# Kernel tuning notes

Measured on AMD Instinct MI355X. Metric: run time of the kernel, lower is better.

## Reference

```python
import jax, jax.numpy as jnp
import numpy as np

N, E_DIM, T = 32, 512, 2048
N_E = 8192
BETA = 0.25

def setup_inputs() -> dict:
    key = jax.random.key(0)
    k1, k2 = jax.random.split(key)
    z = jax.random.normal(k1, (N, E_DIM, T), dtype=jnp.float32)
    # nn.Embedding weight initialized uniform(-1/n_e, 1/n_e)
    emb = jax.random.uniform(k2, (N_E, E_DIM), dtype=jnp.float32,
                             minval=-1.0 / N_E, maxval=1.0 / N_E)
    return {"z": z, "emb": emb}

def reference(z, emb):
    n, width, t = z.shape
    # preprocess: (N, C, T) -> (N, T, C) -> (N*T, C)
    zf = jnp.transpose(z, (0, 2, 1)).reshape(-1, width)  # [M, e_dim]
    # squared euclidean distances: ||z||^2 + ||e||^2 - 2 z e^T
    d = (jnp.sum(zf ** 2, axis=1, keepdims=True)
         + jnp.sum(emb ** 2, axis=1)
         - 2.0 * jnp.matmul(zf, emb.T))  # [M, n_e]
    idx = jnp.argmin(d, axis=1)  # [M]
    z_q = emb[idx]  # [M, e_dim]
    sg = jax.lax.stop_gradient
    loss = jnp.mean((z_q - sg(zf)) ** 2) + BETA * jnp.mean((sg(z_q) - zf) ** 2)
    # straight-through estimator
    z_q = zf + sg(z_q - zf)
    # (N*T, C) -> (N, T, C) -> (N, C, T)
    z_q = jnp.transpose(z_q.reshape(n, t, width), (0, 2, 1))
    # perplexity from codebook usage histogram
    one_hot = jax.nn.one_hot(idx, emb.shape[0], dtype=zf.dtype)  # [M, n_e]
    e_mean = jnp.mean(one_hot, axis=0)
    perplexity = jnp.exp(-jnp.sum(e_mean * jnp.log(e_mean + 1e-10)))
    return (z_q, loss, perplexity)
```

## Files before the change

kernel.cpp:

```cpp
#include <hip/hip_runtime.h>
#include <stdint.h>

#define NE 8192
#define KD 512
#define MT 65536

typedef __attribute__((ext_vector_type(8))) short bf16x8;
typedef __attribute__((ext_vector_type(4))) float f32x4;

union U128 { uint4 u; bf16x8 b; };

#define WS_SUMZ2   0
#define WS_SUMSMIN 4
#define WS_HIST    8
#define WS_ZEROSZ  40960
#define WS_E2      40960
#define WS_IDX     73728
#define WS_EMB16   335872
#define WS_Z16     8724480

__device__ __forceinline__ unsigned int f2bf(float f) {
    union { float f; unsigned int u; } c; c.f = f;
    return (c.u + 0x7FFFu + ((c.u >> 16) & 1u)) >> 16;
}

__device__ __forceinline__ void load_lds16(const void* g, void* l) {
    __builtin_amdgcn_global_load_lds((const __attribute__((address_space(1))) void*)g,
                                     (__attribute__((address_space(3))) void*)l,
                                     16, 0, 0);
}

__global__ void k_embprep(const float* __restrict__ emb,
                          unsigned short* __restrict__ emb16,
                          float* __restrict__ e2) {
    const int code = blockIdx.x;
    const int lane = threadIdx.x;
    const float4* row = (const float4*)(emb + (size_t)code * KD);
    float4 a = row[lane * 2];
    float4 b = row[lane * 2 + 1];
    float s = a.x*a.x + a.y*a.y + a.z*a.z + a.w*a.w
            + b.x*b.x + b.y*b.y + b.z*b.z + b.w*b.w;
    uint4 o;
    o.x = f2bf(a.x) | (f2bf(a.y) << 16);
    o.y = f2bf(a.z) | (f2bf(a.w) << 16);
    o.z = f2bf(b.x) | (f2bf(b.y) << 16);
    o.w = f2bf(b.z) | (f2bf(b.w) << 16);
    ((uint4*)(emb16 + (size_t)code * KD))[lane] = o;
    #pragma unroll
    for (int off = 32; off; off >>= 1) s += __shfl_down(s, off, 64);
    if (lane == 0) e2[code] = s;
}

__global__ void k_zprep(const float* __restrict__ z,
                        unsigned short* __restrict__ z16,
                        float* __restrict__ sumz2) {
    __shared__ float arr[64][65];
    __shared__ float red[4];
    const int tid = threadIdx.x;
    const int n  = blockIdx.z;
    const int c0 = blockIdx.y * 64;
    const int t0 = blockIdx.x * 64;
    const int tl = tid & 63;
    const int cw = tid >> 6;
    const float* base = z + ((size_t)n * KD + c0) * 2048 + t0;
    float s = 0.f;
    #pragma unroll
    for (int u = 0; u < 16; u++) {
        int c = u * 4 + cw;
        float v = base[(size_t)c * 2048 + tl];
        arr[c][tl] = v;
        s += v * v;
    }
    #pragma unroll
    for (int off = 32; off; off >>= 1) s += __shfl_down(s, off, 64);
    if (tl == 0) red[cw] = s;
    __syncthreads();
    if (tid == 0) atomicAdd(sumz2, red[0] + red[1] + red[2] + red[3]);
    #pragma unroll
    for (int iter = 0; iter < 2; iter++) {
        int task = iter * 256 + tid;
        int row = task >> 3;
        int ch  = task & 7;
        float f0 = arr[ch*8+0][row], f1 = arr[ch*8+1][row],
              f2v = arr[ch*8+2][row], f3 = arr[ch*8+3][row],
              f4 = arr[ch*8+4][row], f5 = arr[ch*8+5][row],
              f6 = arr[ch*8+6][row], f7 = arr[ch*8+7][row];
        uint4 o;
        o.x = f2bf(f0) | (f2bf(f1) << 16);
        o.y = f2bf(f2v) | (f2bf(f3) << 16);
        o.z = f2bf(f4) | (f2bf(f5) << 16);
        o.w = f2bf(f6) | (f2bf(f7) << 16);
        *(uint4*)(z16 + ((size_t)(n * 2048 + t0 + row)) * KD + c0 + ch * 8) = o;
    }
}

__global__ __launch_bounds__(512, 2) void k_main(
    const unsigned short* __restrict__ z16,
    const unsigned short* __restrict__ emb16,
    const float* __restrict__ e2,
    int* __restrict__ g_idx,
    int* __restrict__ hist,
    float* __restrict__ sums)
{
    __shared__ __align__(16) unsigned short zt[128 * 512];
    __shared__ __align__(16) unsigned short et[2][256 * 32];

    const int tid  = threadIdx.x;
    const int lane = tid & 63;
    const int w    = tid >> 6;
    const int wm   = w & 1;
    const int wn   = w >> 1;
    const int quad = lane >> 4;
    const int col  = lane & 15;
    const int m0   = blockIdx.x * 128;

    {
        const int r  = tid >> 2;
        const int jb = (tid & 3) << 4;
        const uint4* gz = (const uint4*)(z16 + (size_t)(m0 + r) * KD);
        uint4* zt4w = (uint4*)zt;
        #pragma unroll
        for (int jj = 0; jj < 16; jj++) {
            int j  = jb + jj;
            int js = (j & 56) | ((j ^ r) & 7);
            zt4w[r * 64 + js] = gz[j];
        }
    }

    const int st_nl0 = w * 16 + (lane >> 2);
    const int st_q   = ((lane & 3) - ((st_nl0 >> 1) & 3)) & 3;
    const int st_q8  = st_q * 8;
    unsigned short* st_l0 = &et[0][0] + w * 512 + lane * 8;
    unsigned short* st_l1 = &et[0][0] + 4096 + w * 512 + lane * 8;

    f32x4 acc[4][4];
    #pragma unroll
    for (int mf = 0; mf < 4; mf++)
        #pragma unroll
        for (int nf = 0; nf < 4; nf++)
            acc[mf][nf] = (f32x4){0.f, 0.f, 0.f, 0.f};

    float rbv[4][4]; int rbi[4][4];
    #pragma unroll
    for (int mf = 0; mf < 4; mf++)
        #pragma unroll
        for (int rg = 0; rg < 4; rg++) { rbv[mf][rg] = 3.0e38f; rbi[mf][rg] = 0; }

    int zbase[4], r7[4];
    #pragma unroll
    for (int mf = 0; mf < 4; mf++) {
        int r = wm * 64 + mf * 16 + col;
        zbase[mf] = r * 64;
        r7[mf] = r & 7;
    }
    int bidx[4];
    #pragma unroll
    for (int nf = 0; nf < 4; nf++) {
        int nn = wn * 64 + nf * 16 + col;
        bidx[nf] = nn * 4 + ((quad + (nn >> 1)) & 3);
    }

    const uint4* zt4 = (const uint4*)zt;
    const uint4* et4[2] = { (const uint4*)&et[0][0], (const uint4*)&et[1][0] };

    {
        const unsigned short* g0 = emb16 + ((size_t)(st_nl0) << 9) + st_q8;
        const unsigned short* g1 = emb16 + ((size_t)(128 + st_nl0) << 9) + st_q8;
        load_lds16(g0, st_l0);
        load_lds16(g1, st_l1);
    }

    #pragma unroll 1
    for (int chunk = 0; chunk < 32; chunk++) {
        #pragma unroll
        for (int kk = 0; kk < 16; kk++) {
            __syncthreads();
            const int nxt = chunk * 16 + kk + 1;
            if (nxt < 512) {
                const int nchunk = nxt >> 4, nkk = nxt & 15, nbuf = nxt & 1;
                const size_t koff = (size_t)nkk * 32 + st_q8;
                const unsigned short* g0 = emb16 + (((size_t)(nchunk * 256 + st_nl0)) << 9) + koff;
                const unsigned short* g1 = emb16 + (((size_t)(nchunk * 256 + 128 + st_nl0)) << 9) + koff;
                load_lds16(g0, st_l0 + nbuf * 8192);
                load_lds16(g1, st_l1 + nbuf * 8192);
            }
            const int buf = kk & 1;
            const int jhi  = (kk * 4) & 56;
            const int jlow = ((kk & 1) << 2) | quad;
            bf16x8 af[4], bfv[4];
            #pragma unroll
            for (int mf = 0; mf < 4; mf++) {
                U128 u; u.u = zt4[zbase[mf] + (jhi | (jlow ^ r7[mf]))];
                af[mf] = u.b;
            }
            #pragma unroll
            for (int nf = 0; nf < 4; nf++) {
                U128 u; u.u = et4[buf][bidx[nf]];
                bfv[nf] = u.b;
            }
            #pragma unroll
            for (int mf = 0; mf < 4; mf++)
                #pragma unroll
                for (int nf = 0; nf < 4; nf++)
                    acc[mf][nf] = __builtin_amdgcn_mfma_f32_16x16x32_bf16(
                        af[mf], bfv[nf], acc[mf][nf], 0, 0, 0);
        }
        const int nb = chunk * 256 + wn * 64 + col;
        float e2v[4];
        #pragma unroll
        for (int nf = 0; nf < 4; nf++) e2v[nf] = e2[nb + nf * 16];
        #pragma unroll
        for (int mf = 0; mf < 4; mf++) {
            #pragma unroll
            for (int rg = 0; rg < 4; rg++) {
                float v0 = fmaf(-2.f, acc[mf][0][rg], e2v[0]);
                float v1 = fmaf(-2.f, acc[mf][1][rg], e2v[1]);
                float v2 = fmaf(-2.f, acc[mf][2][rg], e2v[2]);
                float v3 = fmaf(-2.f, acc[mf][3][rg], e2v[3]);
                float bv = v0; int bn = 0;
                if (v1 < bv) { bv = v1; bn = 1; }
                if (v2 < bv) { bv = v2; bn = 2; }
                if (v3 < bv) { bv = v3; bn = 3; }
                if (bv < rbv[mf][rg]) { rbv[mf][rg] = bv; rbi[mf][rg] = nb + (bn << 4); }
            }
            #pragma unroll
            for (int nf = 0; nf < 4; nf++)
                acc[mf][nf] = (f32x4){0.f, 0.f, 0.f, 0.f};
        }
    }

    #pragma unroll
    for (int mf = 0; mf < 4; mf++) {
        #pragma unroll
        for (int rg = 0; rg < 4; rg++) {
            float bv = rbv[mf][rg]; int bi = rbi[mf][rg];
            #pragma unroll
            for (int off = 1; off < 16; off <<= 1) {
                float ov = __shfl_xor(bv, off, 64);
                int   oi = __shfl_xor(bi, off, 64);
                if (ov < bv || (ov == bv && oi < bi)) { bv = ov; bi = oi; }
            }
            rbv[mf][rg] = bv; rbi[mf][rg] = bi;
        }
    }

    __syncthreads();
    float* sv = (float*)&et[0][0];
    int*   si = (int*)(sv + 512);
    if (col == 0) {
        #pragma unroll
        for (int mf = 0; mf < 4; mf++)
            #pragma unroll
            for (int rg = 0; rg < 4; rg++) {
                int rl = wm * 64 + mf * 16 + quad * 4 + rg;
                sv[wn * 128 + rl] = rbv[mf][rg];
                si[wn * 128 + rl] = rbi[mf][rg];
            }
    }
    __syncthreads();
    float myv = 0.f;
    if (tid < 128) {
        float bv = sv[tid]; int bi = si[tid];
        #pragma unroll
        for (int wnn = 1; wnn < 4; wnn++) {
            float ov = sv[wnn * 128 + tid]; int oi = si[wnn * 128 + tid];
            if (ov < bv || (ov == bv && oi < bi)) { bv = ov; bi = oi; }
        }
        g_idx[m0 + tid] = bi;
        atomicAdd(&hist[bi], 1);
        myv = bv;
    }
    #pragma unroll
    for (int off = 32; off; off >>= 1) myv += __shfl_down(myv, off, 64);
    if (lane == 0 && w < 2) atomicAdd(&sums[1], myv);
}

__global__ void k_final(const int* __restrict__ hist,
                        const float* __restrict__ sums,
                        float* __restrict__ out_scalars) {
    __shared__ float red[4];
    const int tid = threadIdx.x;
    float s = 0.f;
    for (int i = tid; i < NE; i += 256) {
        float e = (float)hist[i] * (1.0f / 65536.0f);
        s += e * logf(e + 1e-10f);
    }
    #pragma unroll
    for (int off = 32; off; off >>= 1) s += __shfl_down(s, off, 64);
    if ((tid & 63) == 0) red[tid >> 6] = s;
    __syncthreads();
    if (tid == 0) {
        float total = red[0] + red[1] + red[2] + red[3];
        float perp = expf(-total);
        float loss = 1.25f * (sums[0] + sums[1]) / (65536.0f * 512.0f);
        out_scalars[0] = loss;
        out_scalars[1] = perp;
    }
}

__global__ void k_gather(const float* __restrict__ emb,
                         const int* __restrict__ idx,
                         float* __restrict__ out) {
    __shared__ int ids[256];
    const int n  = blockIdx.y;
    const int t0 = blockIdx.x * 256;
    const int tid = threadIdx.x;
    ids[tid] = idx[n * 2048 + t0 + tid];
    __syncthreads();
    const int tq = tid & 63;
    const int cg = tid >> 6;
    const float* e0 = emb + (size_t)ids[tq * 4 + 0] * KD;
    const float* e1 = emb + (size_t)ids[tq * 4 + 1] * KD;
    const float* e2p = emb + (size_t)ids[tq * 4 + 2] * KD;
    const float* e3 = emb + (size_t)ids[tq * 4 + 3] * KD;
    for (int cb = cg * 4; cb < KD; cb += 16) {
        float4 a = *(const float4*)(e0 + cb);
        float4 b = *(const float4*)(e1 + cb);
        float4 c = *(const float4*)(e2p + cb);
        float4 d = *(const float4*)(e3 + cb);
        float* op = out + ((size_t)(n * KD + cb)) * 2048 + t0 + tq * 4;
        float4 o0 = {a.x, b.x, c.x, d.x};
        float4 o1 = {a.y, b.y, c.y, d.y};
        float4 o2 = {a.z, b.z, c.z, d.z};
        float4 o3 = {a.w, b.w, c.w, d.w};
        *(float4*)(op)        = o0;
        *(float4*)(op + 2048) = o1;
        *(float4*)(op + 4096) = o2;
        *(float4*)(op + 6144) = o3;
    }
}

extern "C" void kernel_launch(void* const* d_in, const int* in_sizes, int n_in,
                              void* d_out, int out_size, void* d_ws, size_t ws_size,
                              hipStream_t stream) {
    (void)in_sizes; (void)n_in; (void)out_size; (void)ws_size;
    const float* z   = (const float*)d_in[0];
    const float* emb = (const float*)d_in[1];
    float* out = (float*)d_out;
    char* ws = (char*)d_ws;

    float*          sums  = (float*)(ws + WS_SUMZ2);
    int*            hist  = (int*)(ws + WS_HIST);
    float*          e2    = (float*)(ws + WS_E2);
    int*            g_idx = (int*)(ws + WS_IDX);
    unsigned short* emb16 = (unsigned short*)(ws + WS_EMB16);
    unsigned short* z16   = (unsigned short*)(ws + WS_Z16);

    hipMemsetAsync(ws, 0, WS_ZEROSZ, stream);

    k_embprep<<<NE, 64, 0, stream>>>(emb, emb16, e2);
    k_zprep<<<dim3(32, 8, 32), 256, 0, stream>>>(z, z16, sums);
    k_main<<<512, 512, 0, stream>>>(z16, emb16, e2, g_idx, hist, sums);
    k_final<<<1, 256, 0, stream>>>(hist, sums, out + 33554432);
    k_gather<<<dim3(8, 32), 256, 0, stream>>>(emb, g_idx, out);
}
```

Before: 919.3 us.

## Software-pipeline codebook staging through registers and prefetch LDS fragments

Replaces the direct global-to-LDS loads of codebook tiles with a four-deep register ring of plain global loads that are written into the double-buffered LDS a couple of steps later. The A and B fragments for the next k-step are read from LDS before the current MFMA block runs, and the MFMAs are wrapped in s_setprio. The e2 loads for the epilogue are hoisted into the k-loop. The aim is to hide global and LDS latency behind MFMA work and cut barrier stalls, at the cost of more VGPRs. The z-prep kernel separately switches to float4 loads.

```diff
diff --git a/kernel.cpp b/kernel.cpp
--- a/kernel.cpp
+++ b/kernel.cpp
@@ -22,12 +22,6 @@
 __device__ __forceinline__ unsigned int f2bf(float f) {
     union { float f; unsigned int u; } c; c.f = f;
     return (c.u + 0x7FFFu + ((c.u >> 16) & 1u)) >> 16;
-}
-
-__device__ __forceinline__ void load_lds16(const void* g, void* l) {
-    __builtin_amdgcn_global_load_lds((const __attribute__((address_space(1))) void*)g,
-                                     (__attribute__((address_space(3))) void*)l,
-                                     16, 0, 0);
 }
 
 __global__ void k_embprep(const float* __restrict__ emb,
@@ -60,20 +54,21 @@
     const int n  = blockIdx.z;
     const int c0 = blockIdx.y * 64;
     const int t0 = blockIdx.x * 64;
-    const int tl = tid & 63;
-    const int cw = tid >> 6;
+    const int tl4 = (tid & 15) * 4;
+    const int cw  = tid >> 4;
     const float* base = z + ((size_t)n * KD + c0) * 2048 + t0;
     float s = 0.f;
     #pragma unroll
-    for (int u = 0; u < 16; u++) {
-        int c = u * 4 + cw;
-        float v = base[(size_t)c * 2048 + tl];
-        arr[c][tl] = v;
-        s += v * v;
+    for (int u = 0; u < 4; u++) {
+        int c = u * 16 + cw;
+        float4 v = *(const float4*)(base + (size_t)c * 2048 + tl4);
+        arr[c][tl4 + 0] = v.x; arr[c][tl4 + 1] = v.y;
+        arr[c][tl4 + 2] = v.z; arr[c][tl4 + 3] = v.w;
+        s += v.x*v.x + v.y*v.y + v.z*v.z + v.w*v.w;
     }
     #pragma unroll
     for (int off = 32; off; off >>= 1) s += __shfl_down(s, off, 64);
-    if (tl == 0) red[cw] = s;
+    if ((tid & 63) == 0) red[tid >> 6] = s;
     __syncthreads();
     if (tid == 0) atomicAdd(sumz2, red[0] + red[1] + red[2] + red[3]);
     #pragma unroll
@@ -114,6 +109,12 @@
     const int col  = lane & 15;
     const int m0   = blockIdx.x * 128;
 
+    const int st_nl0 = w * 16 + (lane >> 2);
+    const int st_q8  = ((((lane & 3) - ((st_nl0 >> 1) & 3)) & 3)) * 8;
+    unsigned short* st_l0 = &et[0][0] + w * 512 + lane * 8;
+    const unsigned short* gst0 = emb16 + ((size_t)st_nl0 << 9) + st_q8;
+    const unsigned short* gst1 = gst0 + (128 << 9);
+
     {
         const int r  = tid >> 2;
         const int jb = (tid & 3) << 4;
@@ -127,11 +128,15 @@
         }
     }
 
-    const int st_nl0 = w * 16 + (lane >> 2);
-    const int st_q   = ((lane & 3) - ((st_nl0 >> 1) & 3)) & 3;
-    const int st_q8  = st_q * 8;
-    unsigned short* st_l0 = &et[0][0] + w * 512 + lane * 8;
-    unsigned short* st_l1 = &et[0][0] + 4096 + w * 512 + lane * 8;
+    uint4 sg0[4], sg1[4];
+    uint4 p00 = *(const uint4*)(gst0);
+    uint4 p01 = *(const uint4*)(gst1);
+    uint4 p10 = *(const uint4*)(gst0 + 32);
+    uint4 p11 = *(const uint4*)(gst1 + 32);
+    sg0[2] = *(const uint4*)(gst0 + 64);
+    sg1[2] = *(const uint4*)(gst1 + 64);
+    sg0[3] = *(const uint4*)(gst0 + 96);
+    sg1[3] = *(const uint4*)(gst1 + 96);
 
     f32x4 acc[4][4];
     #pragma unroll
@@ -160,63 +165,85 @@
         bidx[nf] = nn * 4 + ((quad + (nn >> 1)) & 3);
     }
 
+    *(uint4*)st_l0 = p00;
+    *(uint4*)(st_l0 + 4096) = p01;
+    *(uint4*)(st_l0 + 8192) = p10;
+    *(uint4*)(st_l0 + 12288) = p11;
+    asm volatile("s_waitcnt lgkmcnt(0)" ::: "memory");
+    __builtin_amdgcn_s_barrier();
+
     const uint4* zt4 = (const uint4*)zt;
-    const uint4* et4[2] = { (const uint4*)&et[0][0], (const uint4*)&et[1][0] };
-
-    {
-        const unsigned short* g0 = emb16 + ((size_t)(st_nl0) << 9) + st_q8;
-        const unsigned short* g1 = emb16 + ((size_t)(128 + st_nl0) << 9) + st_q8;
-        load_lds16(g0, st_l0);
-        load_lds16(g1, st_l1);
+
+    bf16x8 af[2][4], bfv[2][4];
+    #pragma unroll
+    for (int mf = 0; mf < 4; mf++) {
+        U128 u; u.u = zt4[zbase[mf] + (quad ^ r7[mf])];
+        af[0][mf] = u.b;
+    }
+    #pragma unroll
+    for (int nf = 0; nf < 4; nf++) {
+        U128 u; u.u = ((const uint4*)&et[0][0])[bidx[nf]];
+        bfv[0][nf] = u.b;
     }
 
     #pragma unroll 1
     for (int chunk = 0; chunk < 32; chunk++) {
+        float e2v0, e2v1, e2v2, e2v3;
         #pragma unroll
         for (int kk = 0; kk < 16; kk++) {
-            __syncthreads();
-            const int nxt = chunk * 16 + kk + 1;
-            if (nxt < 512) {
-                const int nchunk = nxt >> 4, nkk = nxt & 15, nbuf = nxt & 1;
-                const size_t koff = (size_t)nkk * 32 + st_q8;
-                const unsigned short* g0 = emb16 + (((size_t)(nchunk * 256 + st_nl0)) << 9) + koff;
-                const unsigned short* g1 = emb16 + (((size_t)(nchunk * 256 + 128 + st_nl0)) << 9) + koff;
-                load_lds16(g0, st_l0 + nbuf * 8192);
-                load_lds16(g1, st_l1 + nbuf * 8192);
-            }
-            const int buf = kk & 1;
-            const int jhi  = (kk * 4) & 56;
-            const int jlow = ((kk & 1) << 2) | quad;
-            bf16x8 af[4], bfv[4];
-            #pragma unroll
-            for (int mf = 0; mf < 4; mf++) {
-                U128 u; u.u = zt4[zbase[mf] + (jhi | (jlow ^ r7[mf]))];
-                af[mf] = u.b;
-            }
-            #pragma unroll
-            for (int nf = 0; nf < 4; nf++) {
-                U128 u; u.u = et4[buf][bidx[nf]];
-                bfv[nf] = u.b;
-            }
+            const int g = chunk * 16 + kk;
+            {
+                int s = g + 4; if (s > 511) s = 511;
+                const size_t off = (((size_t)(s >> 4)) << 17) + (size_t)((s & 15) * 32);
+                sg0[kk & 3] = *(const uint4*)(gst0 + off);
+                sg1[kk & 3] = *(const uint4*)(gst1 + off);
+            }
+            {
+                const int kk1 = (kk + 1) & 15;
+                const int jhi = (kk1 * 4) & 56;
+                const int jlow = ((kk1 & 1) << 2) | quad;
+                const uint4* etp = (const uint4*)&et[(kk + 1) & 1][0];
+                #pragma unroll
+                for (int mf = 0; mf < 4; mf++) {
+                    U128 u; u.u = zt4[zbase[mf] + (jhi | (jlow ^ r7[mf]))];
+                    af[(kk + 1) & 1][mf] = u.b;
+                }
+                #pragma unroll
+                for (int nf = 0; nf < 4; nf++) {
+                    U128 u; u.u = etp[bidx[nf]];
+                    bfv[(kk + 1) & 1][nf] = u.b;
+                }
+            }
+            {
+                unsigned short* d0 = st_l0 + ((kk & 1) << 13);
+                *(uint4*)d0 = sg0[(kk + 2) & 3];
+                *(uint4*)(d0 + 4096) = sg1[(kk + 2) & 3];
+            }
+            if (kk == 14) {
+                const int nbv = chunk * 256 + wn * 64 + col;
+                e2v0 = e2[nbv];      e2v1 = e2[nbv + 16];
+                e2v2 = e2[nbv + 32]; e2v3 = e2[nbv + 48];
+            }
+            __builtin_amdgcn_s_setprio(1);
             #pragma unroll
             for (int mf = 0; mf < 4; mf++)
                 #pragma unroll
                 for (int nf = 0; nf < 4; nf++)
                     acc[mf][nf] = __builtin_amdgcn_mfma_f32_16x16x32_bf16(
-                        af[mf], bfv[nf], acc[mf][nf], 0, 0, 0);
+                        af[kk & 1][mf], bfv[kk & 1][nf], acc[mf][nf], 0, 0, 0);
+            __builtin_amdgcn_s_setprio(0);
+            asm volatile("s_waitcnt lgkmcnt(0)" ::: "memory");
+            __builtin_amdgcn_s_barrier();
         }
         const int nb = chunk * 256 + wn * 64 + col;
-        float e2v[4];
-        #pragma unroll
-        for (int nf = 0; nf < 4; nf++) e2v[nf] = e2[nb + nf * 16];
         #pragma unroll
         for (int mf = 0; mf < 4; mf++) {
             #pragma unroll
             for (int rg = 0; rg < 4; rg++) {
-                float v0 = fmaf(-2.f, acc[mf][0][rg], e2v[0]);
-                float v1 = fmaf(-2.f, acc[mf][1][rg], e2v[1]);
-                float v2 = fmaf(-2.f, acc[mf][2][rg], e2v[2]);
-                float v3 = fmaf(-2.f, acc[mf][3][rg], e2v[3]);
+                float v0 = fmaf(-2.f, acc[mf][0][rg], e2v0);
+                float v1 = fmaf(-2.f, acc[mf][1][rg], e2v1);
+                float v2 = fmaf(-2.f, acc[mf][2][rg], e2v2);
+                float v3 = fmaf(-2.f, acc[mf][3][rg], e2v3);
                 float bv = v0; int bn = 0;
                 if (v1 < bv) { bv = v1; bn = 1; }
                 if (v2 < bv) { bv = v2; bn = 2; }
```

Result: slower. 1.403 ms (+52.6%).

## Software-pipeline z fragment loads, prefetch e2, and vectorize zprep loads

Applied to the files above, without the earlier changes.

The main distance GEMM loop now double-buffers the A-operand (z) fragments in registers, loading the next k-step's fragments before issuing the current MFMAs. The barrier moves to the end of each iteration. Codebook norms e2 are prefetched during the second-to-last k-step so the per-chunk argmin does not stall on a global load. MFMA issue is bracketed with s_setprio to favour the matrix work, and the z preprocessing kernel switches to float4 global loads. The register double buffer raises VGPR pressure, which may lower occupancy.

```diff
diff --git a/kernel.cpp b/kernel.cpp
--- a/kernel.cpp
+++ b/kernel.cpp
@@ -60,20 +60,21 @@
     const int n  = blockIdx.z;
     const int c0 = blockIdx.y * 64;
     const int t0 = blockIdx.x * 64;
-    const int tl = tid & 63;
-    const int cw = tid >> 6;
+    const int tl4 = (tid & 15) * 4;
+    const int cw  = tid >> 4;
     const float* base = z + ((size_t)n * KD + c0) * 2048 + t0;
     float s = 0.f;
     #pragma unroll
-    for (int u = 0; u < 16; u++) {
-        int c = u * 4 + cw;
-        float v = base[(size_t)c * 2048 + tl];
-        arr[c][tl] = v;
-        s += v * v;
+    for (int u = 0; u < 4; u++) {
+        int c = u * 16 + cw;
+        float4 v = *(const float4*)(base + (size_t)c * 2048 + tl4);
+        arr[c][tl4 + 0] = v.x; arr[c][tl4 + 1] = v.y;
+        arr[c][tl4 + 2] = v.z; arr[c][tl4 + 3] = v.w;
+        s += v.x*v.x + v.y*v.y + v.z*v.z + v.w*v.w;
     }
     #pragma unroll
     for (int off = 32; off; off >>= 1) s += __shfl_down(s, off, 64);
-    if (tl == 0) red[cw] = s;
+    if ((tid & 63) == 0) red[tid >> 6] = s;
     __syncthreads();
     if (tid == 0) atomicAdd(sumz2, red[0] + red[1] + red[2] + red[3]);
     #pragma unroll
@@ -133,36 +134,6 @@
     unsigned short* st_l0 = &et[0][0] + w * 512 + lane * 8;
     unsigned short* st_l1 = &et[0][0] + 4096 + w * 512 + lane * 8;
 
-    f32x4 acc[4][4];
-    #pragma unroll
-    for (int mf = 0; mf < 4; mf++)
-        #pragma unroll
-        for (int nf = 0; nf < 4; nf++)
-            acc[mf][nf] = (f32x4){0.f, 0.f, 0.f, 0.f};
-
-    float rbv[4][4]; int rbi[4][4];
-    #pragma unroll
-    for (int mf = 0; mf < 4; mf++)
-        #pragma unroll
-        for (int rg = 0; rg < 4; rg++) { rbv[mf][rg] = 3.0e38f; rbi[mf][rg] = 0; }
-
-    int zbase[4], r7[4];
-    #pragma unroll
-    for (int mf = 0; mf < 4; mf++) {
-        int r = wm * 64 + mf * 16 + col;
-        zbase[mf] = r * 64;
-        r7[mf] = r & 7;
-    }
-    int bidx[4];
-    #pragma unroll
-    for (int nf = 0; nf < 4; nf++) {
-        int nn = wn * 64 + nf * 16 + col;
-        bidx[nf] = nn * 4 + ((quad + (nn >> 1)) & 3);
-    }
-
-    const uint4* zt4 = (const uint4*)zt;
-    const uint4* et4[2] = { (const uint4*)&et[0][0], (const uint4*)&et[1][0] };
-
     {
         const unsigned short* g0 = emb16 + ((size_t)(st_nl0) << 9) + st_q8;
         const unsigned short* g1 = emb16 + ((size_t)(128 + st_nl0) << 9) + st_q8;
@@ -170,11 +141,51 @@
         load_lds16(g1, st_l1);
     }
 
+    f32x4 acc[4][4];
+    #pragma unroll
+    for (int mf = 0; mf < 4; mf++)
+        #pragma unroll
+        for (int nf = 0; nf < 4; nf++)
+            acc[mf][nf] = (f32x4){0.f, 0.f, 0.f, 0.f};
+
+    float rbv[4][4]; int rbi[4][4];
+    #pragma unroll
+    for (int mf = 0; mf < 4; mf++)
+        #pragma unroll
+        for (int rg = 0; rg < 4; rg++) { rbv[mf][rg] = 3.0e38f; rbi[mf][rg] = 0; }
+
+    int zbase[4], r7[4];
+    #pragma unroll
+    for (int mf = 0; mf < 4; mf++) {
+        int r = wm * 64 + mf * 16 + col;
+        zbase[mf] = r * 64;
+        r7[mf] = r & 7;
+    }
+    int bidx[4];
+    #pragma unroll
+    for (int nf = 0; nf < 4; nf++) {
+        int nn = wn * 64 + nf * 16 + col;
+        bidx[nf] = nn * 4 + ((quad + (nn >> 1)) & 3);
+    }
+
+    const uint4* zt4 = (const uint4*)zt;
+    const uint4* et4[2] = { (const uint4*)&et[0][0], (const uint4*)&et[1][0] };
+
+    __syncthreads();
+
+    bf16x8 afp[2][4];
+    #pragma unroll
+    for (int mf = 0; mf < 4; mf++) {
+        U128 u; u.u = zt4[zbase[mf] + (quad ^ r7[mf])];
+        afp[0][mf] = u.b;
+    }
+
     #pragma unroll 1
     for (int chunk = 0; chunk < 32; chunk++) {
+        float e2v0 = 0.f, e2v1 = 0.f, e2v2 = 0.f, e2v3 = 0.f;
         #pragma unroll
         for (int kk = 0; kk < 16; kk++) {
-            __syncthreads();
+            const int buf = kk & 1;
             const int nxt = chunk * 16 + kk + 1;
             if (nxt < 512) {
                 const int nchunk = nxt >> 4, nkk = nxt & 15, nbuf = nxt & 1;
@@ -184,39 +195,46 @@
                 load_lds16(g0, st_l0 + nbuf * 8192);
                 load_lds16(g1, st_l1 + nbuf * 8192);
             }
-            const int buf = kk & 1;
-            const int jhi  = (kk * 4) & 56;
-            const int jlow = ((kk & 1) << 2) | quad;
-            bf16x8 af[4], bfv[4];
-            #pragma unroll
-            for (int mf = 0; mf < 4; mf++) {
-                U128 u; u.u = zt4[zbase[mf] + (jhi | (jlow ^ r7[mf]))];
-                af[mf] = u.b;
-            }
+            bf16x8 bfv[4];
             #pragma unroll
             for (int nf = 0; nf < 4; nf++) {
                 U128 u; u.u = et4[buf][bidx[nf]];
                 bfv[nf] = u.b;
             }
+            {
+                const int kk1 = (kk + 1) & 15;
+                const int jhi  = (kk1 * 4) & 56;
+                const int jlow = ((kk1 & 1) << 2) | quad;
+                #pragma unroll
+                for (int mf = 0; mf < 4; mf++) {
+                    U128 u; u.u = zt4[zbase[mf] + (jhi | (jlow ^ r7[mf]))];
+                    afp[kk1 & 1][mf] = u.b;
+                }
+            }
+            if (kk == 14) {
+                const int nbv = chunk * 256 + wn * 64 + col;
+                e2v0 = e2[nbv];      e2v1 = e2[nbv + 16];
+                e2v2 = e2[nbv + 32]; e2v3 = e2[nbv + 48];
+            }
+            __builtin_amdgcn_s_setprio(1);
             #pragma unroll
             for (int mf = 0; mf < 4; mf++)
                 #pragma unroll
                 for (int nf = 0; nf < 4; nf++)
                     acc[mf][nf] = __builtin_amdgcn_mfma_f32_16x16x32_bf16(
-                        af[mf], bfv[nf], acc[mf][nf], 0, 0, 0);
+                        afp[buf][mf], bfv[nf], acc[mf][nf], 0, 0, 0);
+            __builtin_amdgcn_s_setprio(0);
+            __syncthreads();
         }
         const int nb = chunk * 256 + wn * 64 + col;
-        float e2v[4];
-        #pragma unroll
-        for (int nf = 0; nf < 4; nf++) e2v[nf] = e2[nb + nf * 16];
         #pragma unroll
         for (int mf = 0; mf < 4; mf++) {
             #pragma unroll
             for (int rg = 0; rg < 4; rg++) {
-                float v0 = fmaf(-2.f, acc[mf][0][rg], e2v[0]);
-                float v1 = fmaf(-2.f, acc[mf][1][rg], e2v[1]);
-                float v2 = fmaf(-2.f, acc[mf][2][rg], e2v[2]);
-                float v3 = fmaf(-2.f, acc[mf][3][rg], e2v[3]);
+                float v0 = fmaf(-2.f, acc[mf][0][rg], e2v0);
+                float v1 = fmaf(-2.f, acc[mf][1][rg], e2v1);
+                float v2 = fmaf(-2.f, acc[mf][2][rg], e2v2);
+                float v3 = fmaf(-2.f, acc[mf][3][rg], e2v3);
                 float bv = v0; int bn = 0;
                 if (v1 < bv) { bv = v1; bn = 1; }
                 if (v2 < bv) { bv = v2; bn = 2; }
```

Result: no change. 929.0 us (+1.1%).
